# Performance work log

Measured on AMD Instinct MI355X. Metric: run time of the kernel, lower is better.

Reference implementation:

```python
import jax, jax.numpy as jnp
import numpy as np

TAU = 6.0       # LIF time constant
VTH = 3.0       # firing threshold
ALPHA = 4.0     # spikingjelly Sigmoid surrogate alpha

@jax.custom_vjp
def heaviside(x):
    # spikingjelly heaviside: 1 if x >= 0 else 0; sigmoid surrogate gradient
    return (x >= 0.0).astype(x.dtype)

def _h_fwd(x):
    return heaviside(x), x

def _h_bwd(x, g):
    s = jax.nn.sigmoid(ALPHA * x)
    return (g * ALPHA * s * (1.0 - s),)

heaviside.defvjp(_h_fwd, _h_bwd)


def setup_inputs() -> dict:
    key = jax.random.key(0)
    k1, k2, k3 = jax.random.split(key, 3)
    B, C, T = 2048, 256, 512
    x = jax.random.normal(k1, (B, C, T), dtype=jnp.float32)
    # init: normal(mean=0.8, std=0.2) clamped to [0, 1] (spiking + WTA branch)
    Wf = jnp.clip(0.8 + 0.2 * jax.random.normal(k2, (C, C), dtype=jnp.float32), 0.0, 1.0)
    Wr = jnp.clip(0.8 + 0.2 * jax.random.normal(k3, (C, C), dtype=jnp.float32), 0.0, 1.0)
    return {"x": x, "Wf": Wf, "Wr": Wr}


def _run(x, Wf, Wr):
    B, C, T = x.shape
    xt = jnp.transpose(x, (2, 0, 1))  # [T, B, C]
    decay = 1.0 - 1.0 / TAU

    def step(carry, x_t):
        v, cache, _ = carry
        # forward_linear is under torch.no_grad() -> stop_gradient
        inp = jax.lax.stop_gradient(x_t @ Wf.T) + cache @ Wr.T
        # LIF charge: decay_input=False, hard reset to v_reset=0
        v = v * decay + inp
        # WTA fire: one-hot argmax mask over channel dim
        mask = jax.nn.one_hot(jnp.argmax(v, axis=1), C, dtype=v.dtype)
        spike_out = heaviside(v * mask - VTH)
        pre_v = v
        # reset uses the UNmasked spike (per WTA_LIFNode.neuronal_reset)
        spike_reset = heaviside(v - VTH)
        v = v * (1.0 - spike_reset)
        return (v, spike_out, pre_v), None

    z = jnp.zeros((B, C), x.dtype)
    (v, cache, pre_v), _ = jax.lax.scan(step, (z, z, z), xt)
    return jnp.exp(pre_v)


def reference(x, Wf, Wr):
    return _run(x, Wf, Wr)
```

## Files before the change

kernel.cpp:

```cpp
#include <hip/hip_runtime.h>
#include <math.h>

#define Bn 2048
#define Cn 256
#define Tn 512
#define VTHf 3.0f

__global__ void transpose_kernel(const float* __restrict__ Wr, float* __restrict__ WrT)
{
    WrT[(size_t)blockIdx.x * Cn + threadIdx.x] =
        Wr[(size_t)threadIdx.x * Cn + blockIdx.x];
}

__global__ __launch_bounds__(256) void gemm_kernel(
    const float* __restrict__ x, const float* __restrict__ Wf,
    float* __restrict__ Y, int t0, int Tc)
{
    const int nTt  = Tc >> 6;
    const int tt   = blockIdx.x % nTt;
    const int cc   = blockIdx.x / nTt;
    const int b    = blockIdx.y;
    const int tbase = t0 + tt * 64;
    const int cbase = cc * 64;

    __shared__ float As[16][64];
    __shared__ float Ws[16][68];

    const int tid = threadIdx.x;
    const int tx  = tid & 15;
    const int ty  = tid >> 4;

    float acc[4][4];
    #pragma unroll
    for (int i = 0; i < 4; ++i)
        #pragma unroll
        for (int j = 0; j < 4; ++j) acc[i][j] = 0.f;

    const float* xb = x + (size_t)b * Cn * Tn;

    const int lt = tid & 63;
    const int lk = tid >> 6;
    const int wk = tid & 15;
    const int wc = tid >> 4;

    for (int k0 = 0; k0 < Cn; k0 += 16) {
        #pragma unroll
        for (int p = 0; p < 4; ++p)
            As[lk + 4 * p][lt] = xb[(size_t)(k0 + lk + 4 * p) * Tn + tbase + lt];
        #pragma unroll
        for (int p = 0; p < 4; ++p)
            Ws[wk][wc + 16 * p] = Wf[(size_t)(cbase + wc + 16 * p) * Cn + k0 + wk];
        __syncthreads();

        #pragma unroll
        for (int kk = 0; kk < 16; ++kk) {
            const float4 a4 = *(const float4*)&As[kk][ty * 4];
            const float4 w4 = *(const float4*)&Ws[kk][tx * 4];
            const float a[4] = {a4.x, a4.y, a4.z, a4.w};
            const float w[4] = {w4.x, w4.y, w4.z, w4.w};
            #pragma unroll
            for (int i = 0; i < 4; ++i)
                #pragma unroll
                for (int j = 0; j < 4; ++j)
                    acc[i][j] = fmaf(a[i], w[j], acc[i][j]);
        }
        __syncthreads();
    }

    float* Yb = Y + ((size_t)b * Tc + (size_t)(tbase - t0)) * Cn + cbase;
    #pragma unroll
    for (int i = 0; i < 4; ++i) {
        float4 o = make_float4(acc[i][0], acc[i][1], acc[i][2], acc[i][3]);
        *(float4*)&Yb[(size_t)(ty * 4 + i) * Cn + tx * 4] = o;
    }
}

__global__ __launch_bounds__(256) void scan_kernel(
    const float* __restrict__ Y, const float* __restrict__ WrT,
    float* __restrict__ vstate, int* __restrict__ jstate,
    float* __restrict__ out, int t0, int t1, int Tc)
{
    const int wave = threadIdx.x >> 6;
    const int lane = threadIdx.x & 63;
    const int b    = blockIdx.x * 4 + wave;
    const int c0   = lane * 4;

    const float DECAY = (float)(1.0 - 1.0 / 6.0);

    float4 v;
    int jf;
    if (t0 == 0) {
        v = make_float4(0.f, 0.f, 0.f, 0.f);
        jf = -1;
    } else {
        v  = *(const float4*)&vstate[(size_t)b * Cn + c0];
        jf = jstate[b];
    }

    const float4* Yb = (const float4*)(Y + (size_t)b * Tc * Cn) + lane;
    float4 ycur = Yb[0];
    float4 pv = v;

    for (int t = t0; t < t1; ++t) {
        float4 ynext;
        if (t + 1 < t1) ynext = Yb[(size_t)(t + 1 - t0) * 64];

        float4 inp = ycur;
        if (jf >= 0) {
            const float4 r = *(const float4*)&WrT[(size_t)jf * Cn + c0];
            inp.x += r.x; inp.y += r.y; inp.z += r.z; inp.w += r.w;
        }
        v.x = __fadd_rn(__fmul_rn(v.x, DECAY), inp.x);
        v.y = __fadd_rn(__fmul_rn(v.y, DECAY), inp.y);
        v.z = __fadd_rn(__fmul_rn(v.z, DECAY), inp.z);
        v.w = __fadd_rn(__fmul_rn(v.w, DECAY), inp.w);

        float mv = v.x; int mi = c0;
        if (v.y > mv) { mv = v.y; mi = c0 + 1; }
        if (v.z > mv) { mv = v.z; mi = c0 + 2; }
        if (v.w > mv) { mv = v.w; mi = c0 + 3; }

        #pragma unroll
        for (int off = 32; off; off >>= 1) {
            float ov = __shfl_xor(mv, off);
            int   oi = __shfl_xor(mi, off);
            if (ov > mv || (ov == mv && oi < mi)) { mv = ov; mi = oi; }
        }
        jf = (mv >= VTHf) ? mi : -1;

        pv = v;
        if (v.x >= VTHf) v.x = 0.f;
        if (v.y >= VTHf) v.y = 0.f;
        if (v.z >= VTHf) v.z = 0.f;
        if (v.w >= VTHf) v.w = 0.f;

        ycur = ynext;
    }

    if (t1 == Tn) {
        float4 o = make_float4(expf(pv.x), expf(pv.y), expf(pv.z), expf(pv.w));
        *(float4*)&out[(size_t)b * Cn + c0] = o;
    } else {
        *(float4*)&vstate[(size_t)b * Cn + c0] = v;
        if (lane == 0) jstate[b] = jf;
    }
}

extern "C" void kernel_launch(void* const* d_in, const int* in_sizes, int n_in,
                              void* d_out, int out_size, void* d_ws, size_t ws_size,
                              hipStream_t stream)
{
    const float* x  = (const float*)d_in[0];
    const float* Wf = (const float*)d_in[1];
    const float* Wr = (const float*)d_in[2];
    float* out = (float*)d_out;

    char* ws = (char*)d_ws;
    float* WrT = (float*)(ws);
    float* vst = (float*)(ws + (size_t)Cn * Cn * 4);
    int*   jst = (int*)  (ws + (size_t)Cn * Cn * 4 + (size_t)Bn * Cn * 4);
    size_t ybase = (size_t)Cn * Cn * 4 + (size_t)Bn * Cn * 4 + (size_t)Bn * 4;
    ybase = (ybase + 255) & ~(size_t)255;
    float* Y = (float*)(ws + ybase);
    size_t avail = ws_size > ybase ? ws_size - ybase : 0;

    int Tc = 64;
    if      ((size_t)Bn * Cn * 512 * 4 <= avail) Tc = 512;
    else if ((size_t)Bn * Cn * 256 * 4 <= avail) Tc = 256;
    else if ((size_t)Bn * Cn * 128 * 4 <= avail) Tc = 128;

    transpose_kernel<<<dim3(Cn), dim3(Cn), 0, stream>>>(Wr, WrT);

    for (int t0 = 0; t0 < Tn; t0 += Tc) {
        dim3 g((unsigned)((Tc >> 6) * 4), (unsigned)Bn);
        gemm_kernel<<<g, 256, 0, stream>>>(x, Wf, Y, t0, Tc);
        scan_kernel<<<dim3(Bn / 4), 256, 0, stream>>>(Y, WrT, vst, jst, out,
                                                      t0, t0 + Tc, Tc);
    }
}
```

Baseline: 3.464 ms.

## Enlarge GEMM tiles with pre-transposed Wf and speed up WTA argmax scan

The GEMM now transposes Wf once and uses 128x128 tiles with 8x8 register blocking and vectorized global loads, raising arithmetic intensity over the old 64x64 tiles. The scan kernel replaces the shuffle-based argmax with DPP, swizzle and permlane max reductions followed by a ballot and readlane to pick the index. It also adds a zero row to WrT so the recurrent add needs no branch, and prefetches Y two steps ahead. The larger register tile risks lower occupancy. The permlane32 inline asm depends on gfx950 support.

```diff
diff --git a/kernel.cpp b/kernel.cpp
--- a/kernel.cpp
+++ b/kernel.cpp
@@ -6,13 +6,89 @@
 #define Tn 512
 #define VTHf 3.0f
 
-__global__ void transpose_kernel(const float* __restrict__ Wr, float* __restrict__ WrT)
-{
-    WrT[(size_t)blockIdx.x * Cn + threadIdx.x] =
-        Wr[(size_t)threadIdx.x * Cn + blockIdx.x];
-}
-
-__global__ __launch_bounds__(256) void gemm_kernel(
+__global__ void transpose_kernel(const float* __restrict__ src,
+                                 float* __restrict__ dst, int zrow)
+{
+    if ((int)blockIdx.x == zrow) {
+        dst[(size_t)blockIdx.x * Cn + threadIdx.x] = 0.f;
+        return;
+    }
+    dst[(size_t)blockIdx.x * Cn + threadIdx.x] =
+        src[(size_t)threadIdx.x * Cn + blockIdx.x];
+}
+
+__global__ __launch_bounds__(256, 4) void gemm_kernel(
+    const float* __restrict__ x, const float* __restrict__ WfT,
+    float* __restrict__ Y, int t0, int Tc)
+{
+    const int nTt = Tc >> 7;
+    const int tt  = blockIdx.x % nTt;
+    const int cc  = blockIdx.x / nTt;
+    const int b   = blockIdx.y;
+    const int tbase = t0 + tt * 128;
+    const int cbase = cc * 128;
+
+    __shared__ float As[16][132];
+    __shared__ float Ws[16][132];
+
+    const int tid = threadIdx.x;
+    const int tx  = tid & 15;
+    const int ty  = tid >> 4;
+
+    const int sk = tid >> 4;
+    const int st = (tid & 15) * 8;
+
+    float acc[8][8];
+    #pragma unroll
+    for (int i = 0; i < 8; ++i)
+        #pragma unroll
+        for (int j = 0; j < 8; ++j) acc[i][j] = 0.f;
+
+    const float* xp = x + (size_t)b * Cn * Tn + tbase + st;
+    const float* wp = WfT + cbase + st;
+
+    for (int k0 = 0; k0 < Cn; k0 += 16) {
+        const float* xs = xp + (size_t)(k0 + sk) * Tn;
+        const float4 a0 = *(const float4*)(xs);
+        const float4 a1 = *(const float4*)(xs + 4);
+        const float* wsrc = wp + (size_t)(k0 + sk) * Cn;
+        const float4 w0 = *(const float4*)(wsrc);
+        const float4 w1 = *(const float4*)(wsrc + 4);
+
+        __syncthreads();
+        *(float4*)&As[sk][st]     = a0;
+        *(float4*)&As[sk][st + 4] = a1;
+        *(float4*)&Ws[sk][st]     = w0;
+        *(float4*)&Ws[sk][st + 4] = w1;
+        __syncthreads();
+
+        #pragma unroll
+        for (int kk = 0; kk < 16; ++kk) {
+            float a[8], w[8];
+            *(float4*)&a[0] = *(const float4*)&As[kk][ty * 8];
+            *(float4*)&a[4] = *(const float4*)&As[kk][ty * 8 + 4];
+            *(float4*)&w[0] = *(const float4*)&Ws[kk][tx * 8];
+            *(float4*)&w[4] = *(const float4*)&Ws[kk][tx * 8 + 4];
+            #pragma unroll
+            for (int i = 0; i < 8; ++i)
+                #pragma unroll
+                for (int j = 0; j < 8; ++j)
+                    acc[i][j] = fmaf(a[i], w[j], acc[i][j]);
+        }
+    }
+
+    float* Yb = Y + ((size_t)b * Tc + (size_t)(tbase - t0 + ty * 8)) * Cn
+                  + cbase + tx * 8;
+    #pragma unroll
+    for (int i = 0; i < 8; ++i) {
+        float4 o0 = make_float4(acc[i][0], acc[i][1], acc[i][2], acc[i][3]);
+        float4 o1 = make_float4(acc[i][4], acc[i][5], acc[i][6], acc[i][7]);
+        *(float4*)&Yb[(size_t)i * Cn]     = o0;
+        *(float4*)&Yb[(size_t)i * Cn + 4] = o1;
+    }
+}
+
+__global__ __launch_bounds__(256) void gemm_kernel64(
     const float* __restrict__ x, const float* __restrict__ Wf,
     float* __restrict__ Y, int t0, int Tc)
 {
@@ -75,6 +151,14 @@
     }
 }
 
+template <int CTRL>
+__device__ __forceinline__ float fmax_dpp(float x)
+{
+    int xi = __builtin_bit_cast(int, x);
+    int yi = __builtin_amdgcn_update_dpp(0, xi, CTRL, 0xF, 0xF, true);
+    return fmaxf(x, __builtin_bit_cast(float, yi));
+}
+
 __global__ __launch_bounds__(256) void scan_kernel(
     const float* __restrict__ Y, const float* __restrict__ WrT,
     float* __restrict__ vstate, int* __restrict__ jstate,
@@ -91,25 +175,30 @@
     int jf;
     if (t0 == 0) {
         v = make_float4(0.f, 0.f, 0.f, 0.f);
-        jf = -1;
+        jf = Cn;
     } else {
         v  = *(const float4*)&vstate[(size_t)b * Cn + c0];
         jf = jstate[b];
     }
 
+    const int nT = t1 - t0;
     const float4* Yb = (const float4*)(Y + (size_t)b * Tc * Cn) + lane;
-    float4 ycur = Yb[0];
+
+    float4 y0 = Yb[0];
+    float4 y1 = Yb[(size_t)(nT > 1 ? 1 : 0) * 64];
+    float4 r  = *((const float4*)(WrT + (size_t)jf * Cn) + lane);
     float4 pv = v;
 
-    for (int t = t0; t < t1; ++t) {
-        float4 ynext;
-        if (t + 1 < t1) ynext = Yb[(size_t)(t + 1 - t0) * 64];
-
-        float4 inp = ycur;
-        if (jf >= 0) {
-            const float4 r = *(const float4*)&WrT[(size_t)jf * Cn + c0];
-            inp.x += r.x; inp.y += r.y; inp.z += r.z; inp.w += r.w;
-        }
+    for (int t = 0; t < nT; ++t) {
+        const int pf = (t + 2 < nT) ? (t + 2) : (nT - 1);
+        float4 y2 = Yb[(size_t)pf * 64];
+
+        float4 inp;
+        inp.x = y0.x + r.x;
+        inp.y = y0.y + r.y;
+        inp.z = y0.z + r.z;
+        inp.w = y0.w + r.w;
+
         v.x = __fadd_rn(__fmul_rn(v.x, DECAY), inp.x);
         v.y = __fadd_rn(__fmul_rn(v.y, DECAY), inp.y);
         v.z = __fadd_rn(__fmul_rn(v.z, DECAY), inp.z);
@@ -120,13 +209,27 @@
         if (v.z > mv) { mv = v.z; mi = c0 + 2; }
         if (v.w > mv) { mv = v.w; mi = c0 + 3; }
 
-        #pragma unroll
-        for (int off = 32; off; off >>= 1) {
-            float ov = __shfl_xor(mv, off);
-            int   oi = __shfl_xor(mi, off);
-            if (ov > mv || (ov == mv && oi < mi)) { mv = ov; mi = oi; }
-        }
-        jf = (mv >= VTHf) ? mi : -1;
+        float g = mv;
+        g = fmax_dpp<0xB1>(g);
+        g = fmax_dpp<0x4E>(g);
+        g = fmax_dpp<0x141>(g);
+        g = fmax_dpp<0x140>(g);
+        {
+            int gi = __builtin_amdgcn_ds_swizzle(
+                __builtin_bit_cast(int, g), 0x401F);
+            g = fmaxf(g, __builtin_bit_cast(float, gi));
+        }
+        {
+            float ga = g, gb = g;
+            asm("v_permlane32_swap_b32 %0, %1" : "+v"(ga), "+v"(gb));
+            g = fmaxf(ga, gb);
+        }
+
+        unsigned long long ball = __ballot(mv == g);
+        int first = __ffsll(ball) - 1;
+        int jr = __builtin_amdgcn_readlane(mi, first);
+        int jsel = (g >= VTHf) ? jr : Cn;
+        jf = __builtin_amdgcn_readfirstlane(jsel);
 
         pv = v;
         if (v.x >= VTHf) v.x = 0.f;
@@ -134,7 +237,9 @@
         if (v.z >= VTHf) v.z = 0.f;
         if (v.w >= VTHf) v.w = 0.f;
 
-        ycur = ynext;
+        r = *((const float4*)(WrT + (size_t)jf * Cn) + lane);
+
+        y0 = y1; y1 = y2;
     }
 
     if (t1 == Tn) {
@@ -156,11 +261,12 @@
     float* out = (float*)d_out;
 
     char* ws = (char*)d_ws;
-    float* WrT = (float*)(ws);
-    float* vst = (float*)(ws + (size_t)Cn * Cn * 4);
-    int*   jst = (int*)  (ws + (size_t)Cn * Cn * 4 + (size_t)Bn * Cn * 4);
-    size_t ybase = (size_t)Cn * Cn * 4 + (size_t)Bn * Cn * 4 + (size_t)Bn * 4;
-    ybase = (ybase + 255) & ~(size_t)255;
+    size_t off = 0;
+    float* WrT = (float*)(ws + off); off += (size_t)(Cn + 1) * Cn * 4;
+    float* WfT = (float*)(ws + off); off += (size_t)Cn * Cn * 4;
+    float* vst = (float*)(ws + off); off += (size_t)Bn * Cn * 4;
+    int*   jst = (int*)  (ws + off); off += (size_t)Bn * 4;
+    size_t ybase = (off + 255) & ~(size_t)255;
     float* Y = (float*)(ws + ybase);
     size_t avail = ws_size > ybase ? ws_size - ybase : 0;
 
@@ -169,11 +275,17 @@
     else if ((size_t)Bn * Cn * 256 * 4 <= avail) Tc = 256;
     else if ((size_t)Bn * Cn * 128 * 4 <= avail) Tc = 128;
 
-    transpose_kernel<<<dim3(Cn), dim3(Cn), 0, stream>>>(Wr, WrT);
+    transpose_kernel<<<dim3(Cn + 1), dim3(Cn), 0, stream>>>(Wr, WrT, Cn);
+    transpose_kernel<<<dim3(Cn),     dim3(Cn), 0, stream>>>(Wf, WfT, -1);
 
     for (int t0 = 0; t0 < Tn; t0 += Tc) {
-        dim3 g((unsigned)((Tc >> 6) * 4), (unsigned)Bn);
-        gemm_kernel<<<g, 256, 0, stream>>>(x, Wf, Y, t0, Tc);
+        if (Tc >= 128) {
+            dim3 g((unsigned)((Tc >> 7) * 2), (unsigned)Bn);
+            gemm_kernel<<<g, 256, 0, stream>>>(x, WfT, Y, t0, Tc);
+        } else {
+            dim3 g((unsigned)((Tc >> 6) * 4), (unsigned)Bn);
+            gemm_kernel64<<<g, 256, 0, stream>>>(x, Wf, Y, t0, Tc);
+        }
         scan_kernel<<<dim3(Bn / 4), 256, 0, stream>>>(Y, WrT, vst, jst, out,
                                                       t0, t0 + Tc, Tc);
     }
```

Result: faster. 2.939 ms (-15.2%).
